# Optimization experiments

Measured on AMD Instinct MI355X. Metric: run time of the kernel, lower is better.

Reference implementation:

```python
import jax, jax.numpy as jnp
import numpy as np

H = 1024   # hidden_size
S = 1024   # seq_length
B = 32     # batch_size


def setup_inputs() -> dict:
    key = jax.random.key(0)
    k1, k2, k3, k4, k5, k6 = jax.random.split(key, 6)
    scale = 1.0 / np.sqrt(3 * H)
    return {
        "encoder_states": jax.random.normal(k1, (S, B, 2 * H), dtype=jnp.float32),
        "hidden": jax.random.normal(k2, (B, H), dtype=jnp.float32),
        "cell": jax.random.normal(k3, (B, H), dtype=jnp.float32),
        "W_attn": jax.random.normal(k4, (H, 3 * H), dtype=jnp.float32) * scale,
        "b_attn": jax.random.normal(k5, (H,), dtype=jnp.float32) * scale,
        "v_w": jax.random.normal(k6, (H,), dtype=jnp.float32) * (1.0 / np.sqrt(H)),
    }


def reference(encoder_states, hidden, cell, W_attn, b_attn, v_w):
    # cell is accepted by the original forward but unused.
    # Split the concat-linear into two projections (mathematically identical,
    # avoids materializing the repeated hidden + concat tensor):
    # cat((hidden_rep, enc), -1) @ W.T == hidden @ W[:, :H].T + enc @ W[:, H:].T
    W_h = W_attn[:, :H]          # [H, H]   multiplies decoder hidden
    W_e = W_attn[:, H:]          # [H, 2H]  multiplies encoder states
    enc = jnp.transpose(encoder_states, (1, 0, 2))          # [B, S, 2H]
    h_proj = hidden @ W_h.T + b_attn                         # [B, H], broadcast over S
    e_proj = jnp.einsum("bse,he->bsh", enc, W_e)             # [B, S, H]
    energy = jnp.tanh(h_proj[:, None, :] + e_proj)           # [B, S, H]
    attention = jnp.einsum("bsh,h->bs", energy, v_w)         # [B, S]
    return jax.nn.softmax(attention, axis=1)
```

## Files before the change

### kernel.cpp

```cpp
#include <hip/hip_runtime.h>
#include <hip/hip_bf16.h>

#define H 1024
#define S 1024
#define B 32
#define K2 2048

typedef unsigned short u16;
typedef __attribute__((ext_vector_type(8))) short short8;
typedef __attribute__((ext_vector_type(8))) unsigned short u16x8;
typedef __attribute__((ext_vector_type(4))) float floatx4;

__device__ __forceinline__ u16 f2bf(float f) {
  unsigned u = __float_as_uint(f);
  u += 0x7FFFu + ((u >> 16) & 1u);
  return (u16)(u >> 16);
}

__device__ __forceinline__ void gld_lds16(const void* g, void* l) {
  __builtin_amdgcn_global_load_lds(
      (const __attribute__((address_space(1))) unsigned int*)g,
      (__attribute__((address_space(3))) unsigned int*)l, 16, 0, 0);
}

__device__ __forceinline__ unsigned cvt_pk(float lo, float hi) {
  __hip_bfloat162 h = __float22bfloat162_rn(float2{lo, hi});
  return *(unsigned*)&h;
}

__device__ __forceinline__ short8 mk_frag(floatx4 lo, floatx4 hi) {
  union { unsigned u[4]; short8 s; } r;
  r.u[0] = cvt_pk(lo[0], lo[1]);
  r.u[1] = cvt_pk(lo[2], lo[3]);
  r.u[2] = cvt_pk(hi[0], hi[1]);
  r.u[3] = cvt_pk(hi[2], hi[3]);
  return r.s;
}

__global__ void conv_we_k(const float* __restrict__ W, u16* __restrict__ dst) {
  const int h = blockIdx.x;
  const int t = threadIdx.x * 8;
  const float* sp = W + (size_t)h * 3072 + H + t;
  u16* dp = dst + (size_t)h * K2 + t;
  floatx4 x = *(const floatx4*)sp;
  floatx4 y = *(const floatx4*)(sp + 4);
  u16x8 o;
  o[0] = f2bf(x[0]); o[1] = f2bf(x[1]); o[2] = f2bf(x[2]); o[3] = f2bf(x[3]);
  o[4] = f2bf(y[0]); o[5] = f2bf(y[1]); o[6] = f2bf(y[2]); o[7] = f2bf(y[3]);
  *(u16x8*)dp = o;
}

__global__ void hproj_k(const float* __restrict__ hidden, const float* __restrict__ W,
                        const float* __restrict__ b_attn, float* __restrict__ hp) {
  const int lane = threadIdx.x & 63;
  const int h = (blockIdx.x * blockDim.x + threadIdx.x) >> 6;
  float wr[16];
#pragma unroll
  for (int i = 0; i < 16; i++) wr[i] = W[(size_t)h * 3072 + lane + i * 64];
  for (int b = 0; b < B; b++) {
    float d = 0.f;
#pragma unroll
    for (int i = 0; i < 16; i++) d = fmaf(wr[i], hidden[b * H + lane + i * 64], d);
#pragma unroll
    for (int off = 32; off; off >>= 1) d += __shfl_xor(d, off);
    if (lane == 0) hp[b * H + h] = d + b_attn[h];
  }
}

#define BM 128
#define BN 128
#define BK 32

__global__ __launch_bounds__(256, 4) void gemm_fused2_k(
    const float* __restrict__ enc,
    const u16* __restrict__ Bw,
    const float* __restrict__ hp, const float* __restrict__ vw,
    float* __restrict__ attn) {
  __shared__ __align__(16) u16 sA[2][BM * BK];
  __shared__ __align__(16) u16 sB[2][BN * BK];
  const int tid = threadIdx.x;
  const int bid = blockIdx.x;
  const int ntile = bid >> 8;
  const int b = (bid & 255) >> 3;
  const int mtile = bid & 7;
  const int s0 = mtile * BM;
  const int h0 = ntile * BN;

  const int lane = tid & 63;
  const int wv = tid >> 6;
  const int wm = (wv >> 1) * 64;
  const int wn = (wv & 1) * 64;
  const int fr = lane & 15;
  const int kgrp = lane >> 4;

  const int ar = tid >> 1;
  const int ah = tid & 1;
  const int asw = (ar >> 1) & 3;
  const float* agp = enc + ((size_t)(s0 + ar) * B + b) * K2 + ah * 16;
  const int aseg0 = ((2 * ah) ^ asw) << 3;
  const int aseg1 = ((2 * ah + 1) ^ asw) << 3;

  const int lr4 = lane >> 2, sg4 = lane & 3;

  floatx4 acc[4][4];
#pragma unroll
  for (int i = 0; i < 4; i++)
#pragma unroll
    for (int j = 0; j < 4; j++) acc[i][j] = (floatx4){0.f, 0.f, 0.f, 0.f};

  floatx4 a0, a1, a2, a3;

  a0 = *(const floatx4*)(agp + 0);
  a1 = *(const floatx4*)(agp + 4);
  a2 = *(const floatx4*)(agp + 8);
  a3 = *(const floatx4*)(agp + 12);
#pragma unroll
  for (int p = 0; p < 2; p++) {
    const int r = wv * 32 + p * 16 + lr4;
    gld_lds16(Bw + (size_t)(h0 + r) * K2 + ((sg4 ^ ((r >> 1) & 3)) << 3),
              (char*)sB[0] + (wv * 32 + p * 16) * 64);
  }
  {
    u16* aw = &sA[0][ar * BK];
    *(short8*)(aw + aseg0) = mk_frag(a0, a1);
    *(short8*)(aw + aseg1) = mk_frag(a2, a3);
  }
  __syncthreads();

  for (int t = 0; t < K2 / BK; ++t) {
    const int c = t & 1;
    const int k1 = (t + 1) * BK;
    if (k1 < K2) {
      const float* ap = agp + k1;
      a0 = *(const floatx4*)(ap + 0);
      a1 = *(const floatx4*)(ap + 4);
      a2 = *(const floatx4*)(ap + 8);
      a3 = *(const floatx4*)(ap + 12);
#pragma unroll
      for (int p = 0; p < 2; p++) {
        const int r = wv * 32 + p * 16 + lr4;
        gld_lds16(Bw + (size_t)(h0 + r) * K2 + k1 + ((sg4 ^ ((r >> 1) & 3)) << 3),
                  (char*)sB[1 - c] + (wv * 32 + p * 16) * 64);
      }
    }
    short8 af[4], bfr[4];
#pragma unroll
    for (int mf = 0; mf < 4; mf++) {
      const int R = wm + mf * 16 + fr;
      af[mf] = *(const short8*)&sA[c][R * BK + ((kgrp ^ ((R >> 1) & 3)) << 3)];
    }
#pragma unroll
    for (int nf = 0; nf < 4; nf++) {
      const int R = wn + nf * 16 + fr;
      bfr[nf] = *(const short8*)&sB[c][R * BK + ((kgrp ^ ((R >> 1) & 3)) << 3)];
    }
#pragma unroll
    for (int mf = 0; mf < 4; mf++)
#pragma unroll
      for (int nf = 0; nf < 4; nf++)
        acc[mf][nf] =
            __builtin_amdgcn_mfma_f32_16x16x32_bf16(af[mf], bfr[nf], acc[mf][nf], 0, 0, 0);
    if (k1 < K2) {
      u16* aw = &sA[1 - c][ar * BK];
      *(short8*)(aw + aseg0) = mk_frag(a0, a1);
      *(short8*)(aw + aseg1) = mk_frag(a2, a3);
    }
    __syncthreads();
  }

  const int col = fr;
  const int rgrp = lane >> 4;
  float hv[4], vv[4];
#pragma unroll
  for (int nf = 0; nf < 4; nf++) {
    const int h = h0 + wn + nf * 16 + col;
    hv[nf] = hp[b * H + h];
    vv[nf] = vw[h];
  }
#pragma unroll
  for (int mf = 0; mf < 4; mf++) {
#pragma unroll
    for (int r = 0; r < 4; r++) {
      float part = 0.f;
#pragma unroll
      for (int nf = 0; nf < 4; nf++) part += tanhf(acc[mf][nf][r] + hv[nf]) * vv[nf];
      part += __shfl_xor(part, 1);
      part += __shfl_xor(part, 2);
      part += __shfl_xor(part, 4);
      part += __shfl_xor(part, 8);
      if (col == 0)
        atomicAdd(&attn[b * S + s0 + wm + mf * 16 + rgrp * 4 + r], part);
    }
  }
}

__global__ void softmax_k(const float* __restrict__ attn, float* __restrict__ out) {
  __shared__ float red[8];
  const int b = blockIdx.x;
  const int tid = threadIdx.x;
  const float* row = attn + b * S;
  float v[4];
#pragma unroll
  for (int i = 0; i < 4; i++) v[i] = row[tid + i * 256];
  float m = fmaxf(fmaxf(v[0], v[1]), fmaxf(v[2], v[3]));
#pragma unroll
  for (int off = 32; off; off >>= 1) m = fmaxf(m, __shfl_xor(m, off));
  if ((tid & 63) == 0) red[tid >> 6] = m;
  __syncthreads();
  m = fmaxf(fmaxf(red[0], red[1]), fmaxf(red[2], red[3]));
  float e[4], sum = 0.f;
#pragma unroll
  for (int i = 0; i < 4; i++) { e[i] = __expf(v[i] - m); sum += e[i]; }
#pragma unroll
  for (int off = 32; off; off >>= 1) sum += __shfl_xor(sum, off);
  __syncthreads();
  if ((tid & 63) == 0) red[4 + (tid >> 6)] = sum;
  __syncthreads();
  sum = red[4] + red[5] + red[6] + red[7];
  const float inv = 1.0f / sum;
#pragma unroll
  for (int i = 0; i < 4; i++) out[b * S + tid + i * 256] = e[i] * inv;
}

extern "C" void kernel_launch(void* const* d_in, const int* in_sizes, int n_in,
                              void* d_out, int out_size, void* d_ws, size_t ws_size,
                              hipStream_t stream) {
  const float* enc    = (const float*)d_in[0];
  const float* hidden = (const float*)d_in[1];
  const float* W_attn = (const float*)d_in[3];
  const float* b_attn = (const float*)d_in[4];
  const float* v_w    = (const float*)d_in[5];
  float* out = (float*)d_out;

  char* ws = (char*)d_ws;
  float* attn = (float*)ws;
  float* hp   = (float*)(ws + 131072);
  u16* Web    = (u16*)(ws + 262144);

  hipMemsetAsync(attn, 0, B * S * sizeof(float), stream);
  conv_we_k<<<H, 256, 0, stream>>>(W_attn, Web);
  hproj_k<<<256, 256, 0, stream>>>(hidden, W_attn, b_attn, hp);
  gemm_fused2_k<<<2048, 256, 0, stream>>>(enc, Web, hp, v_w, attn);
  softmax_k<<<B, 256, 0, stream>>>(attn, out);
}
```

Measured before the change: 620.3 us.

## Pre-convert encoder states to transposed bf16 and stream both GEMM operands via LDS loads

Adds a separate kernel that converts the fp32 encoder states to bf16 in [B,S,2H] order, and changes the GEMM to load A with direct global-to-LDS copies instead of register loads plus in-kernel conversion. The block index mapping is also changed so that N tiles sharing the same A rows are adjacent, and the min-occupancy launch bound is removed. This cuts the GEMM's register traffic and the fp32 A reads, which were repeated for each of the 8 N tiles. The cost is an extra pass that reads 256MB of fp32 and writes 128MB of bf16 through the workspace.

```diff
diff --git a/kernel.cpp b/kernel.cpp
--- a/kernel.cpp
+++ b/kernel.cpp
@@ -21,20 +21,6 @@
   __builtin_amdgcn_global_load_lds(
       (const __attribute__((address_space(1))) unsigned int*)g,
       (__attribute__((address_space(3))) unsigned int*)l, 16, 0, 0);
-}
-
-__device__ __forceinline__ unsigned cvt_pk(float lo, float hi) {
-  __hip_bfloat162 h = __float22bfloat162_rn(float2{lo, hi});
-  return *(unsigned*)&h;
-}
-
-__device__ __forceinline__ short8 mk_frag(floatx4 lo, floatx4 hi) {
-  union { unsigned u[4]; short8 s; } r;
-  r.u[0] = cvt_pk(lo[0], lo[1]);
-  r.u[1] = cvt_pk(lo[2], lo[3]);
-  r.u[2] = cvt_pk(hi[0], hi[1]);
-  r.u[3] = cvt_pk(hi[2], hi[3]);
-  return r.s;
 }
 
 __global__ void conv_we_k(const float* __restrict__ W, u16* __restrict__ dst) {
@@ -50,6 +36,21 @@
   *(u16x8*)dp = o;
 }
 
+__global__ void conv_enc_k(const float* __restrict__ enc, u16* __restrict__ dst) {
+  const int sb = blockIdx.x;
+  const int s = sb >> 5;
+  const int b = sb & 31;
+  const int t = threadIdx.x * 8;
+  const float* sp = enc + (size_t)sb * K2 + t;
+  u16* dp = dst + ((size_t)b * S + s) * K2 + t;
+  floatx4 x = *(const floatx4*)sp;
+  floatx4 y = *(const floatx4*)(sp + 4);
+  u16x8 o;
+  o[0] = f2bf(x[0]); o[1] = f2bf(x[1]); o[2] = f2bf(x[2]); o[3] = f2bf(x[3]);
+  o[4] = f2bf(y[0]); o[5] = f2bf(y[1]); o[6] = f2bf(y[2]); o[7] = f2bf(y[3]);
+  *(u16x8*)dp = o;
+}
+
 __global__ void hproj_k(const float* __restrict__ hidden, const float* __restrict__ W,
                         const float* __restrict__ b_attn, float* __restrict__ hp) {
   const int lane = threadIdx.x & 63;
@@ -71,8 +72,8 @@
 #define BN 128
 #define BK 32
 
-__global__ __launch_bounds__(256, 4) void gemm_fused2_k(
-    const float* __restrict__ enc,
+__global__ __launch_bounds__(256) void gemm_bf16_2ph_k(
+    const u16* __restrict__ A,
     const u16* __restrict__ Bw,
     const float* __restrict__ hp, const float* __restrict__ vw,
     float* __restrict__ attn) {
@@ -80,9 +81,9 @@
   __shared__ __align__(16) u16 sB[2][BN * BK];
   const int tid = threadIdx.x;
   const int bid = blockIdx.x;
-  const int ntile = bid >> 8;
-  const int b = (bid & 255) >> 3;
-  const int mtile = bid & 7;
+  const int ntile = bid & 7;
+  const int mtile = (bid >> 3) & 7;
+  const int b = bid >> 6;
   const int s0 = mtile * BM;
   const int h0 = ntile * BN;
 
@@ -93,37 +94,23 @@
   const int fr = lane & 15;
   const int kgrp = lane >> 4;
 
-  const int ar = tid >> 1;
-  const int ah = tid & 1;
-  const int asw = (ar >> 1) & 3;
-  const float* agp = enc + ((size_t)(s0 + ar) * B + b) * K2 + ah * 16;
-  const int aseg0 = ((2 * ah) ^ asw) << 3;
-  const int aseg1 = ((2 * ah + 1) ^ asw) << 3;
-
   const int lr4 = lane >> 2, sg4 = lane & 3;
 
+  const u16* Abase = A + (size_t)b * S * K2;
+
   floatx4 acc[4][4];
 #pragma unroll
   for (int i = 0; i < 4; i++)
 #pragma unroll
     for (int j = 0; j < 4; j++) acc[i][j] = (floatx4){0.f, 0.f, 0.f, 0.f};
 
-  floatx4 a0, a1, a2, a3;
-
-  a0 = *(const floatx4*)(agp + 0);
-  a1 = *(const floatx4*)(agp + 4);
-  a2 = *(const floatx4*)(agp + 8);
-  a3 = *(const floatx4*)(agp + 12);
 #pragma unroll
   for (int p = 0; p < 2; p++) {
     const int r = wv * 32 + p * 16 + lr4;
+    gld_lds16(Abase + (size_t)(s0 + r) * K2 + ((sg4 ^ ((r >> 1) & 3)) << 3),
+              (char*)sA[0] + (wv * 32 + p * 16) * 64);
     gld_lds16(Bw + (size_t)(h0 + r) * K2 + ((sg4 ^ ((r >> 1) & 3)) << 3),
               (char*)sB[0] + (wv * 32 + p * 16) * 64);
-  }
-  {
-    u16* aw = &sA[0][ar * BK];
-    *(short8*)(aw + aseg0) = mk_frag(a0, a1);
-    *(short8*)(aw + aseg1) = mk_frag(a2, a3);
   }
   __syncthreads();
 
@@ -131,14 +118,11 @@
     const int c = t & 1;
     const int k1 = (t + 1) * BK;
     if (k1 < K2) {
-      const float* ap = agp + k1;
-      a0 = *(const floatx4*)(ap + 0);
-      a1 = *(const floatx4*)(ap + 4);
-      a2 = *(const floatx4*)(ap + 8);
-      a3 = *(const floatx4*)(ap + 12);
 #pragma unroll
       for (int p = 0; p < 2; p++) {
         const int r = wv * 32 + p * 16 + lr4;
+        gld_lds16(Abase + (size_t)(s0 + r) * K2 + k1 + ((sg4 ^ ((r >> 1) & 3)) << 3),
+                  (char*)sA[1 - c] + (wv * 32 + p * 16) * 64);
         gld_lds16(Bw + (size_t)(h0 + r) * K2 + k1 + ((sg4 ^ ((r >> 1) & 3)) << 3),
                   (char*)sB[1 - c] + (wv * 32 + p * 16) * 64);
       }
@@ -160,11 +144,6 @@
       for (int nf = 0; nf < 4; nf++)
         acc[mf][nf] =
             __builtin_amdgcn_mfma_f32_16x16x32_bf16(af[mf], bfr[nf], acc[mf][nf], 0, 0, 0);
-    if (k1 < K2) {
-      u16* aw = &sA[1 - c][ar * BK];
-      *(short8*)(aw + aseg0) = mk_frag(a0, a1);
-      *(short8*)(aw + aseg1) = mk_frag(a2, a3);
-    }
     __syncthreads();
   }
 
@@ -236,10 +215,12 @@
   float* attn = (float*)ws;
   float* hp   = (float*)(ws + 131072);
   u16* Web    = (u16*)(ws + 262144);
+  u16* encb   = (u16*)(ws + 4456448);
 
   hipMemsetAsync(attn, 0, B * S * sizeof(float), stream);
   conv_we_k<<<H, 256, 0, stream>>>(W_attn, Web);
   hproj_k<<<256, 256, 0, stream>>>(hidden, W_attn, b_attn, hp);
-  gemm_fused2_k<<<2048, 256, 0, stream>>>(enc, Web, hp, v_w, attn);
+  conv_enc_k<<<S * B, 256, 0, stream>>>(enc, encb);
+  gemm_bf16_2ph_k<<<2048, 256, 0, stream>>>(encb, Web, hp, v_w, attn);
   softmax_k<<<B, 256, 0, stream>>>(attn, out);
 }
```

After: 631.4 us. Within noise of the previous version (+1.8%).
